# Kernel optimization log

Hardware: AMD Instinct MI355X
Metric: run time of the kernel (lower is better)

## Reference

```python
import jax, jax.numpy as jnp
import numpy as np

B, S, C = 16, 2048, 1024
H = 8            # preference_dim / num_heads
HD = C // H      # head_dim = 128


def setup_inputs() -> dict:
    key = jax.random.key(0)
    ks = jax.random.split(key, 8)
    s1 = 1.0 / np.sqrt(1.0)   # Linear(1, HD) init scale (not critical)
    sh = 1.0 / np.sqrt(HD)
    return {
        "features": jax.random.normal(ks[0], (B, S, C), dtype=jnp.float32),
        "preference": jax.random.normal(ks[1], (B, H), dtype=jnp.float32),
        "Wq": jax.random.uniform(ks[2], (HD, 1), jnp.float32, -s1, s1),
        "bq": jax.random.uniform(ks[3], (HD,), jnp.float32, -s1, s1),
        "Wk": jax.random.uniform(ks[4], (HD, HD), jnp.float32, -sh, sh),
        "bk": jax.random.uniform(ks[5], (HD,), jnp.float32, -sh, sh),
        "Wv": jax.random.uniform(ks[6], (HD, HD), jnp.float32, -sh, sh),
        "bv": jax.random.uniform(ks[7], (HD,), jnp.float32, -sh, sh),
    }


def reference(features, preference, Wq, bq, Wk, bk, Wv, bv):
    b, s, c = features.shape
    h, hd = H, HD
    # query: Linear(1->hd) applied to per-head scalar preference; constant over step
    # q[b,h,d] = preference[b,h] * Wq[d,0] + bq[d]
    q = preference[:, :, None] * Wq[:, 0][None, None, :] + bq  # [B,H,HD]
    f = features.reshape(b, s, h, hd)                          # head slices
    k = jnp.einsum('bshd,ed->bshe', f, Wk) + bk                # [B,S,H,HD]
    v = jnp.einsum('bshd,ed->bshe', f, Wv) + bv                # [B,S,H,HD]
    # original builds [B,S,S] scores per head, but query rows are identical
    # across step, so softmax(q @ k^T) @ v has identical rows; compute once.
    scores = jnp.einsum('bhd,bshd->bhs', q, k)                 # [B,H,S]
    attn = jax.nn.softmax(scores, axis=-1)
    ctx = jnp.einsum('bhs,bshd->bhd', attn, v)                 # [B,H,HD]
    weighted = jnp.broadcast_to(ctx[:, None, :, :], (b, s, h, hd)).reshape(b, s, c)
    return weighted + features
```

## Files before the change

### kernel.cpp

```cpp
#include <hip/hip_runtime.h>
#include <math.h>

#define B 16
#define S 2048
#define C 1024
#define H 8
#define HD 128

__global__ void k1_qk(const float* __restrict__ pref, const float* __restrict__ Wq,
                      const float* __restrict__ bq, const float* __restrict__ Wk,
                      float* __restrict__ qk) {
    int bh = blockIdx.x;
    int d  = threadIdx.x;
    __shared__ float qsh[HD];
    float p = pref[bh];
    qsh[d] = p * Wq[d] + bq[d];
    __syncthreads();
    float s = 0.f;
#pragma unroll 8
    for (int e = 0; e < HD; ++e)
        s += qsh[e] * Wk[e * HD + d];
    qk[bh * HD + d] = s;
}

__global__ __launch_bounds__(256) void k2_pass(
    const float* __restrict__ feat, const float* __restrict__ qk,
    float* __restrict__ pm, float* __restrict__ pl, float* __restrict__ pf,
    int NC, int R) {
    int wg    = blockIdx.x;
    int b     = wg / NC;
    int chunk = wg - b * NC;
    int t     = threadIdx.x;
    int h     = t >> 5;
    int lane32 = t & 31;

    const float4* frow = (const float4*)feat
                       + (size_t)(b * S + chunk * R) * (C / 4) + t;
    float4 qv = ((const float4*)qk)[(b * H + h) * (HD / 4) + lane32];

    float m = -1e30f, l = 0.f;
    float a0 = 0.f, a1 = 0.f, a2 = 0.f, a3 = 0.f;

    for (int s = 0; s < R; ++s) {
        float4 f = frow[(size_t)s * (C / 4)];
        float part = f.x * qv.x + f.y * qv.y + f.z * qv.z + f.w * qv.w;
        part += __shfl_xor(part, 16, 32);
        part += __shfl_xor(part, 8, 32);
        part += __shfl_xor(part, 4, 32);
        part += __shfl_xor(part, 2, 32);
        part += __shfl_xor(part, 1, 32);
        float mn    = fmaxf(m, part);
        float scale = __expf(m - mn);
        float p     = __expf(part - mn);
        l  = l * scale + p;
        a0 = a0 * scale + p * f.x;
        a1 = a1 * scale + p * f.y;
        a2 = a2 * scale + p * f.z;
        a3 = a3 * scale + p * f.w;
        m  = mn;
    }
    if (lane32 == 0) { pm[wg * H + h] = m; pl[wg * H + h] = l; }
    float4 o; o.x = a0; o.y = a1; o.z = a2; o.w = a3;
    ((float4*)pf)[(size_t)wg * (C / 4) + t] = o;
}

__global__ __launch_bounds__(128) void k3_combine(
    const float* __restrict__ pm, const float* __restrict__ pl,
    const float* __restrict__ pf, const float* __restrict__ Wv,
    const float* __restrict__ bv, float* __restrict__ ctx, int NC) {
    int bh = blockIdx.x;
    int b = bh >> 3, h = bh & 7;
    int t = threadIdx.x;
    __shared__ float wsh[64];
    __shared__ float fsh[HD];

    float M = -1e30f;
    for (int i = 0; i < NC; ++i)
        M = fmaxf(M, pm[(b * NC + i) * H + h]);
    if (t < NC) wsh[t] = __expf(pm[(b * NC + t) * H + h] - M);
    __syncthreads();
    float L = 0.f;
    for (int i = 0; i < NC; ++i)
        L += pl[(b * NC + i) * H + h] * wsh[i];
    float acc = 0.f;
    for (int i = 0; i < NC; ++i)
        acc += pf[(size_t)(b * NC + i) * C + h * HD + t] * wsh[i];
    fsh[t] = acc / L;
    __syncthreads();
    float s = 0.f;
#pragma unroll 8
    for (int d = 0; d < HD; ++d)
        s += fsh[d] * Wv[t * HD + d];
    ctx[bh * HD + t] = s + bv[t];
}

__global__ __launch_bounds__(256) void k4_epilogue(
    const float* __restrict__ feat, const float* __restrict__ ctx,
    float* __restrict__ out) {
    size_t i = (size_t)blockIdx.x * blockDim.x + threadIdx.x;
    float4 f = ((const float4*)feat)[i];
    size_t b  = i >> 19;
    size_t c4 = i & 255;
    float4 cv = ((const float4*)ctx)[b * (C / 4) + c4];
    float4 o; o.x = f.x + cv.x; o.y = f.y + cv.y;
    o.z = f.z + cv.z; o.w = f.w + cv.w;
    ((float4*)out)[i] = o;
}

extern "C" void kernel_launch(void* const* d_in, const int* in_sizes, int n_in,
                              void* d_out, int out_size, void* d_ws, size_t ws_size,
                              hipStream_t stream) {
    const float* feat = (const float*)d_in[0];
    const float* pref = (const float*)d_in[1];
    const float* Wq   = (const float*)d_in[2];
    const float* bq   = (const float*)d_in[3];
    const float* Wk   = (const float*)d_in[4];
    const float* Wv   = (const float*)d_in[6];
    const float* bv   = (const float*)d_in[7];
    float* out = (float*)d_out;

    int NC = 64;
    auto need = [](int nc) {
        return (size_t)(B * H * HD + B * C + 2 * B * nc * H + (size_t)B * nc * C) * 4;
    };
    while (NC > 1 && need(NC) > ws_size) NC >>= 1;
    int R = S / NC;

    float* ws  = (float*)d_ws;
    float* qk  = ws;
    float* ctx = qk + B * H * HD;
    float* pm  = ctx + B * C;
    float* pl  = pm + B * NC * H;
    float* pf  = pl + B * NC * H;

    k1_qk<<<B * H, HD, 0, stream>>>(pref, Wq, bq, Wk, qk);
    k2_pass<<<B * NC, 256, 0, stream>>>(feat, qk, pm, pl, pf, NC, R);
    k3_combine<<<B * H, HD, 0, stream>>>(pm, pl, pf, Wv, bv, ctx, NC);
    k4_epilogue<<<(B * S * C / 4) / 256, 256, 0, stream>>>(feat, ctx, out);
}
```

Before: 292.0 us.

## Fuse all stages into one cooperative kernel with grid syncs

Replaces the four launches with a single cooperative kernel of 1024 blocks. Each block computes its own q·Wk vector, runs the online-softmax pass over its chunk of rows, grid-syncs, lets the first 128 blocks combine partials and apply Wv, then grid-syncs again before every block adds ctx to its own rows. The epilogue re-reads the same chunk the block already streamed, which may hit in cache, and writes the output with nontemporal stores. The softmax rescale is now done lazily, only when some lane's score exceeds the running max by more than 8. The gain is fewer launches and possibly better cache reuse, at the cost of two grid-wide barriers and a requirement that all 1024 blocks be co-resident.

```diff
diff --git a/kernel.cpp b/kernel.cpp
--- a/kernel.cpp
+++ b/kernel.cpp
@@ -1,110 +1,113 @@
 #include <hip/hip_runtime.h>
+#include <hip/hip_cooperative_groups.h>
 #include <math.h>
+
+namespace cg = cooperative_groups;
 
 #define B 16
 #define S 2048
 #define C 1024
 #define H 8
 #define HD 128
+#define NC 64
+#define R  (S / NC)
 
-__global__ void k1_qk(const float* __restrict__ pref, const float* __restrict__ Wq,
-                      const float* __restrict__ bq, const float* __restrict__ Wk,
-                      float* __restrict__ qk) {
-    int bh = blockIdx.x;
-    int d  = threadIdx.x;
-    __shared__ float qsh[HD];
-    float p = pref[bh];
-    qsh[d] = p * Wq[d] + bq[d];
-    __syncthreads();
-    float s = 0.f;
-#pragma unroll 8
-    for (int e = 0; e < HD; ++e)
-        s += qsh[e] * Wk[e * HD + d];
-    qk[bh * HD + d] = s;
-}
+typedef float f32x4 __attribute__((ext_vector_type(4)));
 
-__global__ __launch_bounds__(256) void k2_pass(
-    const float* __restrict__ feat, const float* __restrict__ qk,
-    float* __restrict__ pm, float* __restrict__ pl, float* __restrict__ pf,
-    int NC, int R) {
-    int wg    = blockIdx.x;
-    int b     = wg / NC;
-    int chunk = wg - b * NC;
-    int t     = threadIdx.x;
-    int h     = t >> 5;
+__global__ __launch_bounds__(256, 4) void fused(
+    const float* __restrict__ feat, const float* __restrict__ pref,
+    const float* __restrict__ Wq, const float* __restrict__ bq,
+    const float* __restrict__ Wk, const float* __restrict__ Wv,
+    const float* __restrict__ bv, float* __restrict__ out,
+    float* __restrict__ ctx, float* __restrict__ pm,
+    float* __restrict__ pl, float* __restrict__ pf)
+{
+    cg::grid_group grid = cg::this_grid();
+
+    int wg     = blockIdx.x;
+    int b      = wg >> 6;
+    int chunk  = wg & (NC - 1);
+    int t      = threadIdx.x;
+    int h      = t >> 5;
     int lane32 = t & 31;
 
-    const float4* frow = (const float4*)feat
-                       + (size_t)(b * S + chunk * R) * (C / 4) + t;
-    float4 qv = ((const float4*)qk)[(b * H + h) * (HD / 4) + lane32];
+    __shared__ float qsh[2 * HD];
+    __shared__ float fsh[HD];
+
+    if (t < HD) { qsh[t] = Wq[t]; qsh[HD + t] = bq[t]; }
+    __syncthreads();
+    float p = pref[b * H + h];
+    f32x4 qv = {0.f, 0.f, 0.f, 0.f};
+    const f32x4* Wk4 = (const f32x4*)Wk;
+#pragma unroll 4
+    for (int e = 0; e < HD; ++e) {
+        float qe = fmaf(p, qsh[e], qsh[HD + e]);
+        qv += Wk4[e * (HD / 4) + lane32] * qe;
+    }
+
+    const size_t rowbase = (size_t)(b * S + chunk * R) * (C / 4) + t;
+    const f32x4* frow = (const f32x4*)feat + rowbase;
 
     float m = -1e30f, l = 0.f;
-    float a0 = 0.f, a1 = 0.f, a2 = 0.f, a3 = 0.f;
-
+    f32x4 acc = {0.f, 0.f, 0.f, 0.f};
     for (int s = 0; s < R; ++s) {
-        float4 f = frow[(size_t)s * (C / 4)];
+        f32x4 f = frow[(size_t)s * (C / 4)];
         float part = f.x * qv.x + f.y * qv.y + f.z * qv.z + f.w * qv.w;
         part += __shfl_xor(part, 16, 32);
         part += __shfl_xor(part, 8, 32);
         part += __shfl_xor(part, 4, 32);
         part += __shfl_xor(part, 2, 32);
         part += __shfl_xor(part, 1, 32);
-        float mn    = fmaxf(m, part);
-        float scale = __expf(m - mn);
-        float p     = __expf(part - mn);
-        l  = l * scale + p;
-        a0 = a0 * scale + p * f.x;
-        a1 = a1 * scale + p * f.y;
-        a2 = a2 * scale + p * f.z;
-        a3 = a3 * scale + p * f.w;
-        m  = mn;
+        if (__any(part - m > 8.f)) {
+            float mn    = fmaxf(m, part);
+            float scale = __expf(m - mn);
+            l *= scale; acc *= scale;
+            m = mn;
+        }
+        float pe = __expf(part - m);
+        l   += pe;
+        acc += f * pe;
     }
     if (lane32 == 0) { pm[wg * H + h] = m; pl[wg * H + h] = l; }
-    float4 o; o.x = a0; o.y = a1; o.z = a2; o.w = a3;
-    ((float4*)pf)[(size_t)wg * (C / 4) + t] = o;
-}
+    ((f32x4*)pf)[(size_t)wg * (C / 4) + t] = acc;
 
-__global__ __launch_bounds__(128) void k3_combine(
-    const float* __restrict__ pm, const float* __restrict__ pl,
-    const float* __restrict__ pf, const float* __restrict__ Wv,
-    const float* __restrict__ bv, float* __restrict__ ctx, int NC) {
-    int bh = blockIdx.x;
-    int b = bh >> 3, h = bh & 7;
-    int t = threadIdx.x;
-    __shared__ float wsh[64];
-    __shared__ float fsh[HD];
+    __threadfence();
+    grid.sync();
 
-    float M = -1e30f;
-    for (int i = 0; i < NC; ++i)
-        M = fmaxf(M, pm[(b * NC + i) * H + h]);
-    if (t < NC) wsh[t] = __expf(pm[(b * NC + t) * H + h] - M);
-    __syncthreads();
-    float L = 0.f;
-    for (int i = 0; i < NC; ++i)
-        L += pl[(b * NC + i) * H + h] * wsh[i];
-    float acc = 0.f;
-    for (int i = 0; i < NC; ++i)
-        acc += pf[(size_t)(b * NC + i) * C + h * HD + t] * wsh[i];
-    fsh[t] = acc / L;
-    __syncthreads();
-    float s = 0.f;
+    if (wg < B * H) {
+        int b2 = wg >> 3, h2 = wg & 7;
+        if (t < HD) {
+            float M = -1e30f;
+            for (int i = 0; i < NC; ++i)
+                M = fmaxf(M, pm[(b2 * NC + i) * H + h2]);
+            float L = 0.f, a = 0.f;
+            for (int i = 0; i < NC; ++i) {
+                float w = __expf(pm[(b2 * NC + i) * H + h2] - M);
+                L += pl[(b2 * NC + i) * H + h2] * w;
+                a += pf[(size_t)(b2 * NC + i) * C + h2 * HD + t] * w;
+            }
+            fsh[t] = a / L;
+        }
+        __syncthreads();
+        if (t < HD) {
+            float s2 = 0.f;
 #pragma unroll 8
-    for (int d = 0; d < HD; ++d)
-        s += fsh[d] * Wv[t * HD + d];
-    ctx[bh * HD + t] = s + bv[t];
-}
+            for (int d = 0; d < HD; ++d)
+                s2 += fsh[d] * Wv[t * HD + d];
+            ctx[b2 * C + h2 * HD + t] = s2 + bv[t];
+        }
+    }
 
-__global__ __launch_bounds__(256) void k4_epilogue(
-    const float* __restrict__ feat, const float* __restrict__ ctx,
-    float* __restrict__ out) {
-    size_t i = (size_t)blockIdx.x * blockDim.x + threadIdx.x;
-    float4 f = ((const float4*)feat)[i];
-    size_t b  = i >> 19;
-    size_t c4 = i & 255;
-    float4 cv = ((const float4*)ctx)[b * (C / 4) + c4];
-    float4 o; o.x = f.x + cv.x; o.y = f.y + cv.y;
-    o.z = f.z + cv.z; o.w = f.w + cv.w;
-    ((float4*)out)[i] = o;
+    __threadfence();
+    grid.sync();
+
+    f32x4 cvv = ((const f32x4*)ctx)[b * (C / 4) + t];
+    f32x4* orow = (f32x4*)out + rowbase;
+    for (int s = 0; s < R; ++s) {
+        f32x4 f = frow[(size_t)s * (C / 4)];
+        f32x4 o = f + cvv;
+        __builtin_nontemporal_store(o, &orow[(size_t)s * (C / 4)]);
+    }
 }
 
 extern "C" void kernel_launch(void* const* d_in, const int* in_sizes, int n_in,
@@ -119,22 +122,13 @@
     const float* bv   = (const float*)d_in[7];
     float* out = (float*)d_out;
 
-    int NC = 64;
-    auto need = [](int nc) {
-        return (size_t)(B * H * HD + B * C + 2 * B * nc * H + (size_t)B * nc * C) * 4;
-    };
-    while (NC > 1 && need(NC) > ws_size) NC >>= 1;
-    int R = S / NC;
-
-    float* ws  = (float*)d_ws;
-    float* qk  = ws;
-    float* ctx = qk + B * H * HD;
+    float* ctx = (float*)d_ws;
     float* pm  = ctx + B * C;
     float* pl  = pm + B * NC * H;
     float* pf  = pl + B * NC * H;
 
-    k1_qk<<<B * H, HD, 0, stream>>>(pref, Wq, bq, Wk, qk);
-    k2_pass<<<B * NC, 256, 0, stream>>>(feat, qk, pm, pl, pf, NC, R);
-    k3_combine<<<B * H, HD, 0, stream>>>(pm, pl, pf, Wv, bv, ctx, NC);
-    k4_epilogue<<<(B * S * C / 4) / 256, 256, 0, stream>>>(feat, ctx, out);
+    void* args[] = { &feat, &pref, &Wq, &bq, &Wk, &Wv, &bv, &out,
+                     &ctx, &pm, &pl, &pf };
+    hipLaunchCooperativeKernel((const void*)fused, dim3(B * NC), dim3(256),
+                               args, 0, stream);
 }
```

Measured after the change: 654.7 us. 2.24x slower.
